# Kernel tuning notes

Hardware: AMD Instinct MI355X
Metric: run time of the kernel (lower is better)

The kernel has to match this reference:

```python
import jax, jax.numpy as jnp
import numpy as np

DIM = 1024
HEADS = 16
HEAD_DIM = DIM // HEADS
FFN = 4096
EPS = 1e-6


def layernorm(x, a, b):
    # torch: mean, std (unbiased, ddof=1), divide by (std + eps)
    mean = jnp.mean(x, axis=-1, keepdims=True)
    std = jnp.std(x, axis=-1, keepdims=True, ddof=1)
    return a * (x - mean) / (std + EPS) + b


def setup_inputs() -> dict:
    key = jax.random.key(0)
    ks = jax.random.split(key, 8)
    B, S = 2, 2048
    x = jax.random.normal(ks[0], (B, S, DIM), dtype=jnp.float32)
    mask = jnp.zeros((1, 1, S, S), dtype=jnp.float32)
    sc = 0.02
    wq = jax.random.normal(ks[1], (DIM, DIM), jnp.float32) * sc
    wk = jax.random.normal(ks[2], (DIM, DIM), jnp.float32) * sc
    wv = jax.random.normal(ks[3], (DIM, DIM), jnp.float32) * sc
    wo = jax.random.normal(ks[4], (DIM, DIM), jnp.float32) * sc
    w1 = jax.random.normal(ks[5], (FFN, DIM), jnp.float32) * sc
    w2 = jax.random.normal(ks[6], (DIM, FFN), jnp.float32) * sc
    a1 = jnp.ones((DIM,), jnp.float32)
    b1 = jnp.zeros((DIM,), jnp.float32)
    a2 = jnp.ones((DIM,), jnp.float32)
    b2 = jnp.zeros((DIM,), jnp.float32)
    return {"x": x, "mask": mask, "wq": wq, "wk": wk, "wv": wv, "wo": wo,
            "w1": w1, "w2": w2, "a1": a1, "b1": b1, "a2": a2, "b2": b2}


def reference(x, mask, wq, wk, wv, wo, w1, w2, a1, b1, a2, b2):
    B, S, _ = x.shape
    # QKV projections (Linear weight is [out, in]; y = x @ W.T)
    q = (x @ wq.T).reshape(B, S, HEADS, HEAD_DIM).transpose(0, 2, 1, 3)
    k = (x @ wk.T).reshape(B, S, HEADS, HEAD_DIM).transpose(0, 2, 1, 3)
    v = (x @ wv.T).reshape(B, S, HEADS, HEAD_DIM).transpose(0, 2, 1, 3)
    scores = jnp.einsum('bhqd,bhkd->bhqk', q, k) / np.sqrt(HEAD_DIM).astype(np.float32)
    scores = scores + mask
    probs = jax.nn.softmax(scores.astype(jnp.float32), axis=-1).astype(q.dtype)
    attn = jnp.einsum('bhqk,bhkd->bhqd', probs, v)
    attn = attn.transpose(0, 2, 1, 3).reshape(B, S, DIM)
    attn_out = attn @ wo.T
    attn_x = layernorm(x + attn_out, a1, b1)
    # FFN with exact (erf) GELU, matching nn.GELU default
    h = jax.nn.gelu(attn_x @ w1.T, approximate=False)
    ffn_out = h @ w2.T
    return layernorm(attn_x + ffn_out, a2, b2)
```

## Files before the change

### kernel.cpp

```cpp
#include <hip/hip_runtime.h>
#include <math.h>

typedef __bf16 bf16x8 __attribute__((ext_vector_type(8)));
typedef float  f32x4  __attribute__((ext_vector_type(4)));
typedef unsigned short us4 __attribute__((ext_vector_type(4)));

__device__ __forceinline__ unsigned short f2bf(float f) {
    union { float f; unsigned int u; } v; v.f = f;
    return (unsigned short)((v.u + 0x7FFFu + ((v.u >> 16) & 1u)) >> 16);
}
__device__ __forceinline__ float bf2f(unsigned short u) {
    union { unsigned int i; float f; } c; c.i = (unsigned)u << 16;
    return c.f;
}
__device__ __forceinline__ unsigned cvt_pk_bf16(float lo, float hi) {
    unsigned r;
    asm("v_cvt_pk_bf16_f32 %0, %1, %2" : "=v"(r) : "v"(lo), "v"(hi));
    return r;
}
__device__ __forceinline__ float exp2_raw(float x) {
    float r;
    asm("v_exp_f32 %0, %1" : "=v"(r) : "v"(x));
    return r;
}
__device__ __forceinline__ void gload_lds16(const unsigned short* g, unsigned short* l) {
    __builtin_amdgcn_global_load_lds((__attribute__((address_space(1))) void*)(g),
                                     (__attribute__((address_space(3))) void*)(l), 16, 0, 0);
}

__global__ __launch_bounds__(256)
void cast_all(const float* __restrict__ x, const float* __restrict__ wq,
              const float* __restrict__ wk, const float* __restrict__ wv,
              const float* __restrict__ wo, const float* __restrict__ w1,
              const float* __restrict__ w2,
              unsigned short* __restrict__ xb, unsigned short* __restrict__ wqkv,
              unsigned short* __restrict__ wob, unsigned short* __restrict__ w1b,
              unsigned short* __restrict__ w2b) {
    const int b = blockIdx.x;
    const float* src; unsigned short* dst; int off;
    if      (b <  4096) { src = x;  dst = xb;             off = b;         }
    else if (b <  5120) { src = wq; dst = wqkv;           off = b - 4096;  }
    else if (b <  6144) { src = wk; dst = wqkv + 1048576; off = b - 5120;  }
    else if (b <  7168) { src = wv; dst = wqkv + 2097152; off = b - 6144;  }
    else if (b <  8192) { src = wo; dst = wob;            off = b - 7168;  }
    else if (b < 12288) { src = w1; dst = w1b;            off = b - 8192;  }
    else                { src = w2; dst = w2b;            off = b - 12288; }
    const int i = off * 1024 + threadIdx.x * 4;
    const float4 v = *reinterpret_cast<const float4*>(src + i);
    us4 o = { f2bf(v.x), f2bf(v.y), f2bf(v.z), f2bf(v.w) };
    *reinterpret_cast<us4*>(dst + i) = o;
}

template<int EPI>
__global__ __launch_bounds__(256)
void gemm_bt(const unsigned short* __restrict__ A, const unsigned short* __restrict__ B,
             void* __restrict__ Cout, int M, int N, int Kstride, int Kc, int NBY) {
    __shared__ __align__(16) unsigned short lds[2][2][128 * 32];
    const int tid = threadIdx.x;
    const int l   = tid & 63;
    const int w   = tid >> 6;
    const int wg  = blockIdx.x;
    const int swz = (wg & 7) * (gridDim.x >> 3) + (wg >> 3);
    const int bm  = (swz / NBY) * 128;
    const int bn  = (swz % NBY) * 128;
    const int kbase = blockIdx.y * Kc;
    const int wr  = (w >> 1) * 64;
    const int wc  = (w & 1) * 64;
    const int wbase = tid & ~63;

    f32x4 acc[4][4] = {};

    auto stage = [&](int buf, int k0) {
#pragma unroll
        for (int c = 0; c < 2; ++c) {
            const int chunk = c * 256 + tid;
            const int r  = chunk >> 2;
            const int cl = (chunk & 3) ^ ((r >> 1) & 3);
            gload_lds16(A + (size_t)(bm + r) * Kstride + kbase + k0 + cl * 8,
                        &lds[buf][0][(c * 256 + wbase) * 8]);
        }
#pragma unroll
        for (int c = 0; c < 2; ++c) {
            const int chunk = c * 256 + tid;
            const int r  = chunk >> 2;
            const int cl = (chunk & 3) ^ ((r >> 1) & 3);
            gload_lds16(B + (size_t)(bn + r) * Kstride + kbase + k0 + cl * 8,
                        &lds[buf][1][(c * 256 + wbase) * 8]);
        }
    };

    stage(0, 0);
    int cur = 0;
    const int nk = Kc >> 5;
    for (int kt = 0; kt < nk; ++kt) {
        __syncthreads();
        if (kt + 1 < nk) stage(cur ^ 1, (kt + 1) << 5);
        bf16x8 af[4], bfr[4];
#pragma unroll
        for (int i = 0; i < 4; ++i) {
            const int ra = wr + i * 16 + (l & 15);
            const int ca = (l >> 4) ^ ((ra >> 1) & 3);
            af[i]  = *reinterpret_cast<const bf16x8*>(&lds[cur][0][ra * 32 + ca * 8]);
            const int rb = wc + i * 16 + (l & 15);
            const int cb = (l >> 4) ^ ((rb >> 1) & 3);
            bfr[i] = *reinterpret_cast<const bf16x8*>(&lds[cur][1][rb * 32 + cb * 8]);
        }
#pragma unroll
        for (int i = 0; i < 4; ++i)
#pragma unroll
            for (int j = 0; j < 4; ++j)
                acc[i][j] = __builtin_amdgcn_mfma_f32_16x16x32_bf16(af[i], bfr[j], acc[i][j], 0, 0, 0);
        cur ^= 1;
    }

#pragma unroll
    for (int i = 0; i < 4; ++i) {
#pragma unroll
        for (int j = 0; j < 4; ++j) {
#pragma unroll
            for (int r = 0; r < 4; ++r) {
                const int m = bm + wr + i * 16 + ((l >> 4) << 2) + r;
                const int n = bn + wc + j * 16 + (l & 15);
                const float v = acc[i][j][r];
                if (EPI == 1) {
                    unsigned short* C = (unsigned short*)Cout;
                    const int s  = m & 2047;
                    const int bh = ((m >> 11) << 4) | ((n & 1023) >> 6);
                    const int d  = n & 63;
                    if (n < 1024)
                        C[(size_t)(bh * 2048 + s) * 64 + d] = f2bf(v * 0.18033688011112042f);
                    else if (n < 2048)
                        C[(size_t)4194304 + (size_t)(bh * 2048 + s) * 64 + d] = f2bf(v);
                    else
                        C[(size_t)8388608 + ((size_t)bh * 64 + d) * 2048 + s] = f2bf(v);
                } else if (EPI == 2) {
                    const float gl = 0.5f * v * (1.0f + erff(v * 0.70710678118654752f));
                    ((unsigned short*)Cout)[(size_t)m * N + n] = f2bf(gl);
                } else {
                    ((unsigned short*)Cout)[(size_t)blockIdx.y * M * N + (size_t)m * N + n] = f2bf(v);
                }
            }
        }
    }
}

__global__ __launch_bounds__(256)
void attn_kernel(const unsigned short* __restrict__ Q, const unsigned short* __restrict__ Kb,
                 const unsigned short* __restrict__ Vt, unsigned short* __restrict__ out) {
    __shared__ __align__(16) unsigned short kld[2][64 * 64];
    __shared__ __align__(16) unsigned short vld[2][64 * 64];
    __shared__ __align__(16) unsigned short plds[4][2][16][72];
    const int tid = threadIdx.x;
    const int l   = tid & 63;
    const int w   = tid >> 6;
    const int g   = l >> 4;
    const int q15 = l & 15;
    const int bh  = blockIdx.x & 31;
    const int qt  = blockIdx.x >> 5;
    const int q0  = qt * 128 + w * 32;
    const size_t base = (size_t)bh * 2048 * 64;

    bf16x8 qa[2][2];
#pragma unroll
    for (int qg = 0; qg < 2; ++qg) {
        const unsigned short* qp = Q + base + (size_t)(q0 + qg * 16 + q15) * 64 + g * 8;
        qa[qg][0] = *reinterpret_cast<const bf16x8*>(qp);
        qa[qg][1] = *reinterpret_cast<const bf16x8*>(qp + 32);
    }

    bf16x8 ones;
    {
        us4 o1 = { 0x3F80, 0x3F80, 0x3F80, 0x3F80 };
        bf16x8 t;
        *reinterpret_cast<us4*>(&t) = o1;
        *(reinterpret_cast<us4*>(&t) + 1) = o1;
        ones = t;
    }

    f32x4 oacc[2][5] = {};
    float mrun[2] = { -1e30f, -1e30f };

    auto stage = [&](int buf, int k0) {
        const int wb = tid & ~63;
#pragma unroll
        for (int it = 0; it < 2; ++it) {
            const int ci = it * 256 + tid;
            const int r  = ci >> 3;
            const int cs = (ci & 7) ^ (r & 7);
            gload_lds16(Kb + base + (size_t)(k0 + r) * 64 + cs * 8,
                        &kld[buf][(it * 256 + wb) * 8]);
        }
#pragma unroll
        for (int it = 0; it < 2; ++it) {
            const int ci = it * 256 + tid;
            const int r  = ci >> 3;
            const int cs = (ci & 7) ^ (r & 7);
            gload_lds16(Vt + base + (size_t)r * 2048 + k0 + cs * 8,
                        &vld[buf][(it * 256 + wb) * 8]);
        }
    };

    stage(0, 0);
    int cur = 0;
    for (int t = 0; t < 32; ++t) {
        __syncthreads();
        if (t + 1 < 32) stage(cur ^ 1, (t + 1) * 64);

        bf16x8 kf[4][2];
#pragma unroll
        for (int ks = 0; ks < 4; ++ks) {
            const int row = ks * 16 + q15;
            const int sw  = row & 7;
            kf[ks][0] = *reinterpret_cast<const bf16x8*>(&kld[cur][row * 64 + ((g    ) ^ sw) * 8]);
            kf[ks][1] = *reinterpret_cast<const bf16x8*>(&kld[cur][row * 64 + ((4 + g) ^ sw) * 8]);
        }
        f32x4 sac[2][4];
#pragma unroll
        for (int qg = 0; qg < 2; ++qg)
#pragma unroll
            for (int ks = 0; ks < 4; ++ks) {
                f32x4 z = { 0.f, 0.f, 0.f, 0.f };
                z = __builtin_amdgcn_mfma_f32_16x16x32_bf16(kf[ks][0], qa[qg][0], z, 0, 0, 0);
                z = __builtin_amdgcn_mfma_f32_16x16x32_bf16(kf[ks][1], qa[qg][1], z, 0, 0, 0);
                sac[qg][ks] = z;
            }

#pragma unroll
        for (int qg = 0; qg < 2; ++qg) {
            float tm = fmaxf(fmaxf(sac[qg][0][0], sac[qg][0][1]), fmaxf(sac[qg][0][2], sac[qg][0][3]));
#pragma unroll
            for (int ks = 1; ks < 4; ++ks) {
                const float a = fmaxf(sac[qg][ks][0], sac[qg][ks][1]);
                const float b = fmaxf(sac[qg][ks][2], sac[qg][ks][3]);
                tm = fmaxf(tm, fmaxf(a, b));
            }
            tm = fmaxf(tm, __shfl_xor(tm, 16));
            tm = fmaxf(tm, __shfl_xor(tm, 32));
            const bool skip = __all(tm <= mrun[qg] + 8.0f);
            const float mnew = skip ? mrun[qg] : fmaxf(mrun[qg], tm);
#pragma unroll
            for (int ks = 0; ks < 4; ++ks) {
                const float p0 = exp2_raw(sac[qg][ks][0] - mnew);
                const float p1 = exp2_raw(sac[qg][ks][1] - mnew);
                const float p2 = exp2_raw(sac[qg][ks][2] - mnew);
                const float p3 = exp2_raw(sac[qg][ks][3] - mnew);
                uint2 pk;
                pk.x = cvt_pk_bf16(p0, p1);
                pk.y = cvt_pk_bf16(p2, p3);
                *reinterpret_cast<uint2*>(&plds[w][qg][q15][ks * 16 + g * 4]) = pk;
            }
            if (!skip) {
                const float sc = exp2_raw(mrun[qg] - mnew);
                float scr[4];
#pragma unroll
                for (int r = 0; r < 4; ++r) scr[r] = __shfl(sc, (l & 48) | (g * 4 + r));
#pragma unroll
                for (int j = 0; j < 5; ++j)
#pragma unroll
                    for (int r = 0; r < 4; ++r) oacc[qg][j][r] *= scr[r];
                mrun[qg] = mnew;
            }
        }

        bf16x8 pa[2][2];
#pragma unroll
        for (int qg = 0; qg < 2; ++qg) {
            pa[qg][0] = *reinterpret_cast<const bf16x8*>(&plds[w][qg][q15][g * 8]);
            pa[qg][1] = *reinterpret_cast<const bf16x8*>(&plds[w][qg][q15][32 + g * 8]);
        }
#pragma unroll
        for (int j = 0; j < 4; ++j) {
            const int row = j * 16 + q15;
            const int sw  = row & 7;
            const bf16x8 v0 = *reinterpret_cast<const bf16x8*>(&vld[cur][row * 64 + ((g    ) ^ sw) * 8]);
            const bf16x8 v1 = *reinterpret_cast<const bf16x8*>(&vld[cur][row * 64 + ((4 + g) ^ sw) * 8]);
#pragma unroll
            for (int qg = 0; qg < 2; ++qg) {
                oacc[qg][j] = __builtin_amdgcn_mfma_f32_16x16x32_bf16(pa[qg][0], v0, oacc[qg][j], 0, 0, 0);
                oacc[qg][j] = __builtin_amdgcn_mfma_f32_16x16x32_bf16(pa[qg][1], v1, oacc[qg][j], 0, 0, 0);
            }
        }
#pragma unroll
        for (int qg = 0; qg < 2; ++qg) {
            oacc[qg][4] = __builtin_amdgcn_mfma_f32_16x16x32_bf16(pa[qg][0], ones, oacc[qg][4], 0, 0, 0);
            oacc[qg][4] = __builtin_amdgcn_mfma_f32_16x16x32_bf16(pa[qg][1], ones, oacc[qg][4], 0, 0, 0);
        }
        cur ^= 1;
    }

    const int b = bh >> 4, h = bh & 15;
#pragma unroll
    for (int qg = 0; qg < 2; ++qg)
#pragma unroll
        for (int r = 0; r < 4; ++r) {
            const float inv = 1.f / oacc[qg][4][r];
            const int q = q0 + qg * 16 + g * 4 + r;
#pragma unroll
            for (int j = 0; j < 4; ++j)
                out[(size_t)(b * 2048 + q) * 1024 + h * 64 + j * 16 + q15] = f2bf(oacc[qg][j][r] * inv);
        }
}

template<int NP>
__global__ __launch_bounds__(256)
void ln_res(const float* __restrict__ X, const unsigned short* __restrict__ P,
            const float* __restrict__ gamma, const float* __restrict__ beta,
            float* __restrict__ o32, unsigned short* __restrict__ o16) {
    __shared__ float red[4];
    const int t = threadIdx.x;
    const size_t row = blockIdx.x;
    const float4 a = *reinterpret_cast<const float4*>(X + row * 1024 + t * 4);
    float v0 = a.x, v1 = a.y, v2 = a.z, v3 = a.w;
#pragma unroll
    for (int p = 0; p < NP; ++p) {
        const us4 rr = *reinterpret_cast<const us4*>(P + (size_t)p * 4194304 + row * 1024 + t * 4);
        v0 += bf2f(rr.x); v1 += bf2f(rr.y); v2 += bf2f(rr.z); v3 += bf2f(rr.w);
    }
    float s = v0 + v1 + v2 + v3;
#pragma unroll
    for (int o = 1; o < 64; o <<= 1) s += __shfl_xor(s, o);
    if ((t & 63) == 0) red[t >> 6] = s;
    __syncthreads();
    const float mean = (red[0] + red[1] + red[2] + red[3]) * (1.f / 1024.f);
    v0 -= mean; v1 -= mean; v2 -= mean; v3 -= mean;
    float q = v0 * v0 + v1 * v1 + v2 * v2 + v3 * v3;
#pragma unroll
    for (int o = 1; o < 64; o <<= 1) q += __shfl_xor(q, o);
    __syncthreads();
    if ((t & 63) == 0) red[t >> 6] = q;
    __syncthreads();
    const float var = (red[0] + red[1] + red[2] + red[3]) * (1.f / 1023.f);
    const float inv = 1.f / (sqrtf(var) + 1e-6f);
    const float4 g  = *reinterpret_cast<const float4*>(gamma + t * 4);
    const float4 be = *reinterpret_cast<const float4*>(beta + t * 4);
    const float y0 = g.x * v0 * inv + be.x;
    const float y1 = g.y * v1 * inv + be.y;
    const float y2 = g.z * v2 * inv + be.z;
    const float y3 = g.w * v3 * inv + be.w;
    float4 o4; o4.x = y0; o4.y = y1; o4.z = y2; o4.w = y3;
    *reinterpret_cast<float4*>(o32 + row * 1024 + t * 4) = o4;
    if (o16) {
        us4 ob = { f2bf(y0), f2bf(y1), f2bf(y2), f2bf(y3) };
        *reinterpret_cast<us4*>(o16 + row * 1024 + t * 4) = ob;
    }
}

extern "C" void kernel_launch(void* const* d_in, const int* in_sizes, int n_in,
                              void* d_out, int out_size, void* d_ws, size_t ws_size,
                              hipStream_t stream) {
    const float* x  = (const float*)d_in[0];
    const float* wq = (const float*)d_in[2];
    const float* wk = (const float*)d_in[3];
    const float* wv = (const float*)d_in[4];
    const float* wo = (const float*)d_in[5];
    const float* w1 = (const float*)d_in[6];
    const float* w2 = (const float*)d_in[7];
    const float* a1 = (const float*)d_in[8];
    const float* b1 = (const float*)d_in[9];
    const float* a2 = (const float*)d_in[10];
    const float* b2 = (const float*)d_in[11];

    char* ws = (char*)d_ws;
    const size_t MB = 1024 * 1024;
    unsigned short* xb      = (unsigned short*)(ws);
    unsigned short* wqkv    = (unsigned short*)(ws + 8  * MB);
    unsigned short* wob     = (unsigned short*)(ws + 14 * MB);
    unsigned short* hbuf    = (unsigned short*)(ws);
    unsigned short* w1b     = (unsigned short*)(ws + 32 * MB);
    unsigned short* w2b     = (unsigned short*)(ws + 40 * MB);
    unsigned short* qkv     = (unsigned short*)(ws + 48 * MB);
    unsigned short* attn    = (unsigned short*)(ws + 72 * MB);
    unsigned short* ffn2p   = (unsigned short*)(ws + 48 * MB);
    unsigned short* projp   = (unsigned short*)(ws + 80 * MB);
    float*          attn_x  = (float*)(ws + 96 * MB);
    unsigned short* attn_xb = (unsigned short*)(ws + 112 * MB);

    cast_all<<<16384, 256, 0, stream>>>(x, wq, wk, wv, wo, w1, w2, xb, wqkv, wob, w1b, w2b);
    gemm_bt<1><<<dim3(768, 1), 256, 0, stream>>>(xb, wqkv, qkv, 4096, 3072, 1024, 1024, 24);
    attn_kernel<<<512, 256, 0, stream>>>(qkv, qkv + 4194304, qkv + 8388608, attn);
    gemm_bt<3><<<dim3(256, 1), 256, 0, stream>>>(attn, wob, projp, 4096, 1024, 1024, 1024, 8);
    ln_res<1><<<4096, 256, 0, stream>>>(x, projp, a1, b1, attn_x, attn_xb);
    gemm_bt<2><<<dim3(1024, 1), 256, 0, stream>>>(attn_xb, w1b, hbuf, 4096, 4096, 1024, 1024, 32);
    gemm_bt<3><<<dim3(256, 4), 256, 0, stream>>>(hbuf, w2b, ffn2p, 4096, 1024, 4096, 1024, 8);
    ln_res<4><<<4096, 256, 0, stream>>>(attn_x, ffn2p, a2, b2, (float*)d_out, nullptr);
}
```

Baseline: 268.9 us.

## Use 256-row GEMM tiles with triple-buffered LDS and 8-wave attention blocks

Replaces the 128x128 double-buffered GEMM with a 512-thread kernel using 256xBN tiles, a three-stage LDS pipeline with explicit vmcnt waits, a new swizzle and raised MFMA priority. The out-projection now uses split-K, and its partial sums are reduced inside the following layernorm. The attention kernel moves to 8 waves of 16 query rows each, with single-chunk K/V staging. These changes aim for more reuse per tile and better overlap of loads with compute, at the cost of higher register pressure and fewer blocks for the smaller GEMMs.

New measurement: 271.9 us. No clear change (+1.1%).

```diff
diff --git a/kernel.cpp b/kernel.cpp
--- a/kernel.cpp
+++ b/kernel.cpp
@@ -51,77 +51,96 @@
     *reinterpret_cast<us4*>(dst + i) = o;
 }
 
-template<int EPI>
-__global__ __launch_bounds__(256)
-void gemm_bt(const unsigned short* __restrict__ A, const unsigned short* __restrict__ B,
+template<int NBI, int EPI>
+__global__ __launch_bounds__(512, 2)
+void gemm256(const unsigned short* __restrict__ A, const unsigned short* __restrict__ B,
              void* __restrict__ Cout, int M, int N, int Kstride, int Kc, int NBY) {
-    __shared__ __align__(16) unsigned short lds[2][2][128 * 32];
+    constexpr int BN = NBI * 128;
+    constexpr int NI = NBI * 2;
+    __shared__ __align__(16) unsigned short Al[3][256 * 32];
+    __shared__ __align__(16) unsigned short Bl[3][BN * 32];
     const int tid = threadIdx.x;
     const int l   = tid & 63;
     const int w   = tid >> 6;
     const int wg  = blockIdx.x;
     const int swz = (wg & 7) * (gridDim.x >> 3) + (wg >> 3);
-    const int bm  = (swz / NBY) * 128;
-    const int bn  = (swz % NBY) * 128;
+    const int bm  = (swz / NBY) * 256;
+    const int bn  = (swz % NBY) * BN;
     const int kbase = blockIdx.y * Kc;
-    const int wr  = (w >> 1) * 64;
-    const int wc  = (w & 1) * 64;
+    const int wr  = w >> 2;
+    const int wc  = w & 3;
     const int wbase = tid & ~63;
 
-    f32x4 acc[4][4] = {};
-
-    auto stage = [&](int buf, int k0) {
-#pragma unroll
-        for (int c = 0; c < 2; ++c) {
-            const int chunk = c * 256 + tid;
-            const int r  = chunk >> 2;
-            const int cl = (chunk & 3) ^ ((r >> 1) & 3);
-            gload_lds16(A + (size_t)(bm + r) * Kstride + kbase + k0 + cl * 8,
-                        &lds[buf][0][(c * 256 + wbase) * 8]);
-        }
-#pragma unroll
-        for (int c = 0; c < 2; ++c) {
-            const int chunk = c * 256 + tid;
-            const int r  = chunk >> 2;
-            const int cl = (chunk & 3) ^ ((r >> 1) & 3);
-            gload_lds16(B + (size_t)(bn + r) * Kstride + kbase + k0 + cl * 8,
-                        &lds[buf][1][(c * 256 + wbase) * 8]);
+    f32x4 acc[8][NI] = {};
+
+    auto stage = [&](int buf, int kt) {
+        const int k0 = kbase + kt * 32;
+#pragma unroll
+        for (int i = 0; i < 2; ++i) {
+            const int ci = i * 512 + tid;
+            const int r  = ci >> 2;
+            const int cl = (ci & 3) ^ (r & 3) ^ ((r >> 2) & 1);
+            gload_lds16(A + (size_t)(bm + r) * Kstride + k0 + cl * 8,
+                        &Al[buf][(i * 512 + wbase) * 8]);
+        }
+#pragma unroll
+        for (int i = 0; i < NBI; ++i) {
+            const int ci = i * 512 + tid;
+            const int r  = ci >> 2;
+            const int cl = (ci & 3) ^ (r & 3) ^ ((r >> 2) & 1);
+            gload_lds16(B + (size_t)(bn + r) * Kstride + k0 + cl * 8,
+                        &Bl[buf][(i * 512 + wbase) * 8]);
         }
     };
 
+    const int nk = Kc >> 5;
     stage(0, 0);
-    int cur = 0;
-    const int nk = Kc >> 5;
+    stage(1, 1);
+    asm volatile("s_waitcnt vmcnt(%0)" :: "n"(2 + NBI) : "memory");
+    __builtin_amdgcn_s_barrier();
+
     for (int kt = 0; kt < nk; ++kt) {
-        __syncthreads();
-        if (kt + 1 < nk) stage(cur ^ 1, (kt + 1) << 5);
-        bf16x8 af[4], bfr[4];
-#pragma unroll
-        for (int i = 0; i < 4; ++i) {
-            const int ra = wr + i * 16 + (l & 15);
-            const int ca = (l >> 4) ^ ((ra >> 1) & 3);
-            af[i]  = *reinterpret_cast<const bf16x8*>(&lds[cur][0][ra * 32 + ca * 8]);
-            const int rb = wc + i * 16 + (l & 15);
-            const int cb = (l >> 4) ^ ((rb >> 1) & 3);
-            bfr[i] = *reinterpret_cast<const bf16x8*>(&lds[cur][1][rb * 32 + cb * 8]);
-        }
-#pragma unroll
-        for (int i = 0; i < 4; ++i)
-#pragma unroll
-            for (int j = 0; j < 4; ++j)
-                acc[i][j] = __builtin_amdgcn_mfma_f32_16x16x32_bf16(af[i], bfr[j], acc[i][j], 0, 0, 0);
-        cur ^= 1;
-    }
-
-#pragma unroll
-    for (int i = 0; i < 4; ++i) {
-#pragma unroll
-        for (int j = 0; j < 4; ++j) {
-#pragma unroll
-            for (int r = 0; r < 4; ++r) {
-                const int m = bm + wr + i * 16 + ((l >> 4) << 2) + r;
-                const int n = bn + wc + j * 16 + (l & 15);
-                const float v = acc[i][j][r];
+        const int cur = kt % 3;
+        if (kt + 2 < nk) stage((kt + 2) % 3, kt + 2);
+        bf16x8 af[8], bfr[NI];
+#pragma unroll
+        for (int mi = 0; mi < 8; ++mi) {
+            const int r  = wr * 128 + mi * 16 + (l & 15);
+            const int cl = (l >> 4) ^ (r & 3) ^ ((r >> 2) & 1);
+            af[mi] = *reinterpret_cast<const bf16x8*>(&Al[cur][r * 32 + cl * 8]);
+        }
+#pragma unroll
+        for (int ni = 0; ni < NI; ++ni) {
+            const int r  = wc * (NI * 16) + ni * 16 + (l & 15);
+            const int cl = (l >> 4) ^ (r & 3) ^ ((r >> 2) & 1);
+            bfr[ni] = *reinterpret_cast<const bf16x8*>(&Bl[cur][r * 32 + cl * 8]);
+        }
+        __builtin_amdgcn_s_setprio(1);
+#pragma unroll
+        for (int mi = 0; mi < 8; ++mi)
+#pragma unroll
+            for (int ni = 0; ni < NI; ++ni)
+                acc[mi][ni] = __builtin_amdgcn_mfma_f32_16x16x32_bf16(af[mi], bfr[ni], acc[mi][ni], 0, 0, 0);
+        __builtin_amdgcn_s_setprio(0);
+        if (kt + 1 < nk) {
+            if (kt + 2 < nk) {
+                asm volatile("s_waitcnt vmcnt(%0)" :: "n"(2 + NBI) : "memory");
+            } else {
+                asm volatile("s_waitcnt vmcnt(0)" ::: "memory");
+            }
+            __builtin_amdgcn_s_barrier();
+        }
+    }
+
+#pragma unroll
+    for (int mi = 0; mi < 8; ++mi) {
+#pragma unroll
+        for (int ni = 0; ni < NI; ++ni) {
+#pragma unroll
+            for (int rr = 0; rr < 4; ++rr) {
+                const int m = bm + wr * 128 + mi * 16 + ((l >> 4) << 2) + rr;
+                const int n = bn + wc * (NI * 16) + ni * 16 + (l & 15);
+                const float v = acc[mi][ni][rr];
                 if (EPI == 1) {
                     unsigned short* C = (unsigned short*)Cout;
                     const int s  = m & 2047;
@@ -144,12 +163,12 @@
     }
 }
 
-__global__ __launch_bounds__(256)
+__global__ __launch_bounds__(512, 4)
 void attn_kernel(const unsigned short* __restrict__ Q, const unsigned short* __restrict__ Kb,
                  const unsigned short* __restrict__ Vt, unsigned short* __restrict__ out) {
     __shared__ __align__(16) unsigned short kld[2][64 * 64];
     __shared__ __align__(16) unsigned short vld[2][64 * 64];
-    __shared__ __align__(16) unsigned short plds[4][2][16][72];
+    __shared__ __align__(16) unsigned short plds[8][16][72];
     const int tid = threadIdx.x;
     const int l   = tid & 63;
     const int w   = tid >> 6;
@@ -157,15 +176,14 @@
     const int q15 = l & 15;
     const int bh  = blockIdx.x & 31;
     const int qt  = blockIdx.x >> 5;
-    const int q0  = qt * 128 + w * 32;
+    const int q0  = qt * 128 + w * 16;
     const size_t base = (size_t)bh * 2048 * 64;
 
-    bf16x8 qa[2][2];
-#pragma unroll
-    for (int qg = 0; qg < 2; ++qg) {
-        const unsigned short* qp = Q + base + (size_t)(q0 + qg * 16 + q15) * 64 + g * 8;
-        qa[qg][0] = *reinterpret_cast<const bf16x8*>(qp);
-        qa[qg][1] = *reinterpret_cast<const bf16x8*>(qp + 32);
+    bf16x8 qa0, qa1;
+    {
+        const unsigned short* qp = Q + base + (size_t)(q0 + q15) * 64 + g * 8;
+        qa0 = *reinterpret_cast<const bf16x8*>(qp);
+        qa1 = *reinterpret_cast<const bf16x8*>(qp + 32);
     }
 
     bf16x8 ones;
@@ -177,27 +195,14 @@
         ones = t;
     }
 
-    f32x4 oacc[2][5] = {};
-    float mrun[2] = { -1e30f, -1e30f };
+    f32x4 oacc[5] = {};
+    float mrun = -1e30f;
 
     auto stage = [&](int buf, int k0) {
-        const int wb = tid & ~63;
-#pragma unroll
-        for (int it = 0; it < 2; ++it) {
-            const int ci = it * 256 + tid;
-            const int r  = ci >> 3;
-            const int cs = (ci & 7) ^ (r & 7);
-            gload_lds16(Kb + base + (size_t)(k0 + r) * 64 + cs * 8,
-                        &kld[buf][(it * 256 + wb) * 8]);
-        }
-#pragma unroll
-        for (int it = 0; it < 2; ++it) {
-            const int ci = it * 256 + tid;
-            const int r  = ci >> 3;
-            const int cs = (ci & 7) ^ (r & 7);
-            gload_lds16(Vt + base + (size_t)r * 2048 + k0 + cs * 8,
-                        &vld[buf][(it * 256 + wb) * 8]);
-        }
+        const int r  = tid >> 3;
+        const int cs = (tid & 7) ^ (r & 7);
+        gload_lds16(Kb + base + (size_t)(k0 + r) * 64 + cs * 8, &kld[buf][(tid & ~63) * 8]);
+        gload_lds16(Vt + base + (size_t)r * 2048 + k0 + cs * 8, &vld[buf][(tid & ~63) * 8]);
     };
 
     stage(0, 0);
@@ -214,91 +219,74 @@
             kf[ks][0] = *reinterpret_cast<const bf16x8*>(&kld[cur][row * 64 + ((g    ) ^ sw) * 8]);
             kf[ks][1] = *reinterpret_cast<const bf16x8*>(&kld[cur][row * 64 + ((4 + g) ^ sw) * 8]);
         }
-        f32x4 sac[2][4];
-#pragma unroll
-        for (int qg = 0; qg < 2; ++qg)
-#pragma unroll
-            for (int ks = 0; ks < 4; ++ks) {
-                f32x4 z = { 0.f, 0.f, 0.f, 0.f };
-                z = __builtin_amdgcn_mfma_f32_16x16x32_bf16(kf[ks][0], qa[qg][0], z, 0, 0, 0);
-                z = __builtin_amdgcn_mfma_f32_16x16x32_bf16(kf[ks][1], qa[qg][1], z, 0, 0, 0);
-                sac[qg][ks] = z;
-            }
-
-#pragma unroll
-        for (int qg = 0; qg < 2; ++qg) {
-            float tm = fmaxf(fmaxf(sac[qg][0][0], sac[qg][0][1]), fmaxf(sac[qg][0][2], sac[qg][0][3]));
-#pragma unroll
-            for (int ks = 1; ks < 4; ++ks) {
-                const float a = fmaxf(sac[qg][ks][0], sac[qg][ks][1]);
-                const float b = fmaxf(sac[qg][ks][2], sac[qg][ks][3]);
-                tm = fmaxf(tm, fmaxf(a, b));
-            }
-            tm = fmaxf(tm, __shfl_xor(tm, 16));
-            tm = fmaxf(tm, __shfl_xor(tm, 32));
-            const bool skip = __all(tm <= mrun[qg] + 8.0f);
-            const float mnew = skip ? mrun[qg] : fmaxf(mrun[qg], tm);
-#pragma unroll
-            for (int ks = 0; ks < 4; ++ks) {
-                const float p0 = exp2_raw(sac[qg][ks][0] - mnew);
-                const float p1 = exp2_raw(sac[qg][ks][1] - mnew);
-                const float p2 = exp2_raw(sac[qg][ks][2] - mnew);
-                const float p3 = exp2_raw(sac[qg][ks][3] - mnew);
-                uint2 pk;
-                pk.x = cvt_pk_bf16(p0, p1);
-                pk.y = cvt_pk_bf16(p2, p3);
-                *reinterpret_cast<uint2*>(&plds[w][qg][q15][ks * 16 + g * 4]) = pk;
-            }
-            if (!skip) {
-                const float sc = exp2_raw(mrun[qg] - mnew);
-                float scr[4];
-#pragma unroll
-                for (int r = 0; r < 4; ++r) scr[r] = __shfl(sc, (l & 48) | (g * 4 + r));
-#pragma unroll
-                for (int j = 0; j < 5; ++j)
-#pragma unroll
-                    for (int r = 0; r < 4; ++r) oacc[qg][j][r] *= scr[r];
-                mrun[qg] = mnew;
-            }
-        }
-
-        bf16x8 pa[2][2];
-#pragma unroll
-        for (int qg = 0; qg < 2; ++qg) {
-            pa[qg][0] = *reinterpret_cast<const bf16x8*>(&plds[w][qg][q15][g * 8]);
-            pa[qg][1] = *reinterpret_cast<const bf16x8*>(&plds[w][qg][q15][32 + g * 8]);
-        }
+        f32x4 sac[4];
+#pragma unroll
+        for (int ks = 0; ks < 4; ++ks) {
+            f32x4 z = { 0.f, 0.f, 0.f, 0.f };
+            z = __builtin_amdgcn_mfma_f32_16x16x32_bf16(kf[ks][0], qa0, z, 0, 0, 0);
+            z = __builtin_amdgcn_mfma_f32_16x16x32_bf16(kf[ks][1], qa1, z, 0, 0, 0);
+            sac[ks] = z;
+        }
+
+        float tm = fmaxf(fmaxf(sac[0][0], sac[0][1]), fmaxf(sac[0][2], sac[0][3]));
+#pragma unroll
+        for (int ks = 1; ks < 4; ++ks) {
+            const float a = fmaxf(sac[ks][0], sac[ks][1]);
+            const float b = fmaxf(sac[ks][2], sac[ks][3]);
+            tm = fmaxf(tm, fmaxf(a, b));
+        }
+        tm = fmaxf(tm, __shfl_xor(tm, 16));
+        tm = fmaxf(tm, __shfl_xor(tm, 32));
+        const bool skip = __all(tm <= mrun + 8.0f);
+        const float mnew = skip ? mrun : fmaxf(mrun, tm);
+#pragma unroll
+        for (int ks = 0; ks < 4; ++ks) {
+            const float p0 = exp2_raw(sac[ks][0] - mnew);
+            const float p1 = exp2_raw(sac[ks][1] - mnew);
+            const float p2 = exp2_raw(sac[ks][2] - mnew);
+            const float p3 = exp2_raw(sac[ks][3] - mnew);
+            uint2 pk;
+            pk.x = cvt_pk_bf16(p0, p1);
+            pk.y = cvt_pk_bf16(p2, p3);
+            *reinterpret_cast<uint2*>(&plds[w][q15][ks * 16 + g * 4]) = pk;
+        }
+        if (!skip) {
+            const float sc = exp2_raw(mrun - mnew);
+            float scr[4];
+#pragma unroll
+            for (int r = 0; r < 4; ++r) scr[r] = __shfl(sc, (l & 48) | (g * 4 + r));
+#pragma unroll
+            for (int j = 0; j < 5; ++j)
+#pragma unroll
+                for (int r = 0; r < 4; ++r) oacc[j][r] *= scr[r];
+            mrun = mnew;
+        }
+
+        const bf16x8 pa0 = *reinterpret_cast<const bf16x8*>(&plds[w][q15][g * 8]);
+        const bf16x8 pa1 = *reinterpret_cast<const bf16x8*>(&plds[w][q15][32 + g * 8]);
 #pragma unroll
         for (int j = 0; j < 4; ++j) {
             const int row = j * 16 + q15;
             const int sw  = row & 7;
             const bf16x8 v0 = *reinterpret_cast<const bf16x8*>(&vld[cur][row * 64 + ((g    ) ^ sw) * 8]);
             const bf16x8 v1 = *reinterpret_cast<const bf16x8*>(&vld[cur][row * 64 + ((4 + g) ^ sw) * 8]);
-#pragma unroll
-            for (int qg = 0; qg < 2; ++qg) {
-                oacc[qg][j] = __builtin_amdgcn_mfma_f32_16x16x32_bf16(pa[qg][0], v0, oacc[qg][j], 0, 0, 0);
-                oacc[qg][j] = __builtin_amdgcn_mfma_f32_16x16x32_bf16(pa[qg][1], v1, oacc[qg][j], 0, 0, 0);
-            }
-        }
-#pragma unroll
-        for (int qg = 0; qg < 2; ++qg) {
-            oacc[qg][4] = __builtin_amdgcn_mfma_f32_16x16x32_bf16(pa[qg][0], ones, oacc[qg][4], 0, 0, 0);
-            oacc[qg][4] = __builtin_amdgcn_mfma_f32_16x16x32_bf16(pa[qg][1], ones, oacc[qg][4], 0, 0, 0);
-        }
+            oacc[j] = __builtin_amdgcn_mfma_f32_16x16x32_bf16(pa0, v0, oacc[j], 0, 0, 0);
+            oacc[j] = __builtin_amdgcn_mfma_f32_16x16x32_bf16(pa1, v1, oacc[j], 0, 0, 0);
+        }
+        oacc[4] = __builtin_amdgcn_mfma_f32_16x16x32_bf16(pa0, ones, oacc[4], 0, 0, 0);
+        oacc[4] = __builtin_amdgcn_mfma_f32_16x16x32_bf16(pa1, ones, oacc[4], 0, 0, 0);
         cur ^= 1;
     }
 
     const int b = bh >> 4, h = bh & 15;
 #pragma unroll
-    for (int qg = 0; qg < 2; ++qg)
-#pragma unroll
-        for (int r = 0; r < 4; ++r) {
-            const float inv = 1.f / oacc[qg][4][r];
-            const int q = q0 + qg * 16 + g * 4 + r;
-#pragma unroll
-            for (int j = 0; j < 4; ++j)
-                out[(size_t)(b * 2048 + q) * 1024 + h * 64 + j * 16 + q15] = f2bf(oacc[qg][j][r] * inv);
-        }
+    for (int r = 0; r < 4; ++r) {
+        const float inv = 1.f / oacc[4][r];
+        const int q = q0 + g * 4 + r;
+#pragma unroll
+        for (int j = 0; j < 4; ++j)
+            out[(size_t)(b * 2048 + q) * 1024 + h * 64 + j * 16 + q15] = f2bf(oacc[j][r] * inv);
+    }
 }
 
 template<int NP>
@@ -369,18 +357,18 @@
     unsigned short* w1b     = (unsigned short*)(ws + 32 * MB);
     unsigned short* w2b     = (unsigned short*)(ws + 40 * MB);
     unsigned short* qkv     = (unsigned short*)(ws + 48 * MB);
-    unsigned short* attn    = (unsigned short*)(ws + 72 * MB);
+    unsigned short* projp   = (unsigned short*)(ws + 48 * MB);
     unsigned short* ffn2p   = (unsigned short*)(ws + 48 * MB);
-    unsigned short* projp   = (unsigned short*)(ws + 80 * MB);
-    float*          attn_x  = (float*)(ws + 96 * MB);
-    unsigned short* attn_xb = (unsigned short*)(ws + 112 * MB);
+    unsigned short* attn    = (unsigned short*)(ws + 80 * MB);
+    float*          attn_x  = (float*)(ws + 88 * MB);
+    unsigned short* attn_xb = (unsigned short*)(ws + 104 * MB);
 
     cast_all<<<16384, 256, 0, stream>>>(x, wq, wk, wv, wo, w1, w2, xb, wqkv, wob, w1b, w2b);
-    gemm_bt<1><<<dim3(768, 1), 256, 0, stream>>>(xb, wqkv, qkv, 4096, 3072, 1024, 1024, 24);
-    attn_kernel<<<512, 256, 0, stream>>>(qkv, qkv + 4194304, qkv + 8388608, attn);
-    gemm_bt<3><<<dim3(256, 1), 256, 0, stream>>>(attn, wob, projp, 4096, 1024, 1024, 1024, 8);
-    ln_res<1><<<4096, 256, 0, stream>>>(x, projp, a1, b1, attn_x, attn_xb);
-    gemm_bt<2><<<dim3(1024, 1), 256, 0, stream>>>(attn_xb, w1b, hbuf, 4096, 4096, 1024, 1024, 32);
-    gemm_bt<3><<<dim3(256, 4), 256, 0, stream>>>(hbuf, w2b, ffn2p, 4096, 1024, 4096, 1024, 8);
+    gemm256<1, 1><<<dim3(384, 1), 512, 0, stream>>>(xb, wqkv, qkv, 4096, 3072, 1024, 1024, 24);
+    attn_kernel<<<512, 512, 0, stream>>>(qkv, qkv + 4194304, qkv + 8388608, attn);
+    gemm256<2, 3><<<dim3(64, 4), 512, 0, stream>>>(attn, wob, projp, 4096, 1024, 1024, 256, 4);
+    ln_res<4><<<4096, 256, 0, stream>>>(x, projp, a1, b1, attn_x, attn_xb);
+    gemm256<2, 2><<<dim3(256, 1), 512, 0, stream>>>(attn_xb, w1b, hbuf, 4096, 4096, 1024, 1024, 16);
+    gemm256<2, 3><<<dim3(64, 4), 512, 0, stream>>>(hbuf, w2b, ffn2p, 4096, 1024, 4096, 1024, 4);
     ln_res<4><<<4096, 256, 0, stream>>>(attn_x, ffn2p, a2, b2, (float*)d_out, nullptr);
 }
```
